# Kernel tuning notes

Measured on AMD Instinct MI355X. Metric: run time of the kernel, lower is better.

Reference implementation:

```python
import jax, jax.numpy as jnp
import numpy as np

N = 50000          # nodes per node type
E = 1_600_000      # edges per canonical etype (avg degree 32)
IN_F = 385         # BERT_EMBEDDING_DIM(384) + NUMERICAL_FEATURES(1)
H = 128            # HIDDEN_DIM
# ntype order: 0=Policy, 1=Control, 2=ComplianceRequirement, 3=Risk
# etypes (src_ntype, dst_ntype): implements, mitigates, violates, addresses, informs
ETYPES = [(0, 1), (1, 3), (3, 2), (0, 2), (2, 0)]


def setup_inputs() -> dict:
    key = jax.random.key(0)
    ks = jax.random.split(key, 12)
    inp = {}
    names = ["feat_policy", "feat_control", "feat_compliance", "feat_risk"]
    for i, n in enumerate(names):
        inp[n] = jax.random.normal(ks[i], (N, IN_F), jnp.float32)
    inp["src"] = jax.random.randint(ks[4], (5, E), 0, N, jnp.int32)
    inp["dst"] = jax.random.randint(ks[5], (5, E), 0, N, jnp.int32)
    s_in = 1.0 / np.sqrt(IN_F).astype(np.float32)
    s_h = np.sqrt(6.0 / (H + H)).astype(np.float32)  # xavier_uniform for GraphConv
    inp["Wp"] = jax.random.uniform(ks[6], (4, IN_F, H), jnp.float32, -s_in, s_in)
    inp["bp"] = jax.random.uniform(ks[7], (4, H), jnp.float32, -s_in, s_in)
    inp["Wc1"] = jax.random.uniform(ks[8], (5, H, H), jnp.float32, -s_h, s_h)
    inp["bc1"] = jnp.zeros((5, H), jnp.float32)
    inp["Wc2"] = jax.random.uniform(ks[9], (5, H, H), jnp.float32, -s_h, s_h)
    inp["bc2"] = jnp.zeros((5, H), jnp.float32)
    return inp


def _graph_conv(x, s, d, W, b):
    """DGL GraphConv(norm='both'): D_dst^{-1/2} A D_src^{-1/2} X W + b."""
    ones = jnp.ones(s.shape[0], x.dtype)
    deg_out = jnp.clip(jax.ops.segment_sum(ones, s, num_segments=N), 1.0)
    deg_in = jnp.clip(jax.ops.segment_sum(ones, d, num_segments=N), 1.0)
    xs = x * jax.lax.rsqrt(deg_out)[:, None]            # [N, H] scale by src out-deg
    agg = jax.ops.segment_sum(xs[s], d, num_segments=N)  # gather + scatter-sum [N, H]
    agg = agg * jax.lax.rsqrt(deg_in)[:, None]
    return agg @ W + b


def reference(feat_policy, feat_control, feat_compliance, feat_risk,
              src, dst, Wp, bp, Wc1, bc1, Wc2, bc2):
    feats = [feat_policy, feat_control, feat_compliance, feat_risk]
    # input projections + relu per node type
    h = [jax.nn.relu(f @ Wp[i] + bp[i]) for i, f in enumerate(feats)]

    def hetero_layer(h, Wc, bc):
        out = [jnp.zeros((N, H), h[0].dtype) for _ in range(4)]
        for k, (st, dt) in enumerate(ETYPES):  # HeteroGraphConv aggregate='sum'
            out[dt] = out[dt] + _graph_conv(h[st], src[k], dst[k], Wc[k], bc[k])
        return out

    h = [jax.nn.relu(v) for v in hetero_layer(h, Wc1, bc1)]
    h = [jax.nn.relu(v) for v in hetero_layer(h, Wc2, bc2)]
    return jnp.stack(h)  # [4, N, H] final embeddings per node type
```

## Files before the change

kernel.cpp:

```cpp
#include <hip/hip_runtime.h>
#include <hip/hip_bf16.h>

#define INF 385
#define HD 128
#define NWG 16
#define HIST_BLOCKS (10 * NWG)

typedef __attribute__((ext_vector_type(8))) short short8;
typedef __attribute__((ext_vector_type(4))) float f32x4;

__device__ inline unsigned short f2b(float f) {
    __hip_bfloat16 h = __float2bfloat16(f);
    return *reinterpret_cast<unsigned short*>(&h);
}
__device__ inline float b2f(unsigned int lo16) {
    union { unsigned int u; float f; } c; c.u = lo16 << 16; return c.f;
}

__device__ __forceinline__ void convert_body(
    const float* f0, const float* f1, const float* f2, const float* f3,
    unsigned int* featB, float* alast, int N, int gid, int nthr)
{
    int per = N * 192;
    int tot = 4 * per;
    for (int p = gid; p < tot; p += nthr) {
        int t = p / per, rem = p - t * per;
        int n = rem / 192, c2 = (rem - n * 192) * 2;
        const float* f = (t < 2) ? (t == 0 ? f0 : f1) : (t == 2 ? f2 : f3);
        const float* row = f + (size_t)n * INF;
        float a = row[c2], b = row[c2 + 1];
        featB[p] = ((unsigned int)f2b(b) << 16) | f2b(a);
    }
    for (int p = gid; p < 4 * N; p += nthr) {
        int t = p / N, n = p - t * N;
        const float* f = (t < 2) ? (t == 0 ? f0 : f1) : (t == 2 ? f2 : f3);
        alast[p] = f[(size_t)n * INF + 384];
    }
}

__global__ __launch_bounds__(1024) void hist_conv_kernel(
    const int* __restrict__ src_all, const int* __restrict__ dst_all,
    unsigned short* __restrict__ partial,
    unsigned short* __restrict__ rank_local,
    int E, int N,
    const float* __restrict__ f0, const float* __restrict__ f1,
    const float* __restrict__ f2, const float* __restrict__ f3,
    unsigned int* __restrict__ featB, float* __restrict__ alast)
{
    __shared__ unsigned int cnt[25000];
    int tid = threadIdx.x;
    if (blockIdx.x >= HIST_BLOCKS) {
        int nconv = gridDim.x - HIST_BLOCKS;
        convert_body(f0, f1, f2, f3, featB, alast, N,
                     (blockIdx.x - HIST_BLOCKS) * 1024 + tid, nconv * 1024);
        return;
    }
    int g = blockIdx.x / NWG;
    int w = blockIdx.x % NWG;
    int half = (N + 1) / 2;
    for (int i = tid; i < half; i += 1024) cnt[i] = 0;
    __syncthreads();

    int C = (E + NWG - 1) / NWG;
    int lo = w * C, hi = min(lo + C, E);
    if (g < 5) {
        const int* arr = dst_all + (size_t)g * E;
        for (int e = lo + tid; e < hi; e += 1024) {
            int d = __builtin_nontemporal_load(&arr[e]);
            unsigned int sh = (d & 1) * 16;
            unsigned int old = atomicAdd(&cnt[d >> 1], 1u << sh);
            rank_local[(size_t)g * E + e] = (unsigned short)((old >> sh) & 0xffffu);
        }
    } else {
        const int* arr = src_all + (size_t)(g - 5) * E;
        for (int e = lo + tid; e < hi; e += 1024) {
            int d = __builtin_nontemporal_load(&arr[e]);
            atomicAdd(&cnt[d >> 1], 1u << ((d & 1) * 16));
        }
    }
    __syncthreads();
    unsigned short* outp = partial + ((size_t)g * NWG + w) * N;
    for (int n = tid; n < N; n += 1024)
        outp[n] = (unsigned short)((cnt[n >> 1] >> ((n & 1) * 16)) & 0xffffu);
}

__global__ void reduce_kernel(unsigned short* __restrict__ partial, int* __restrict__ cnt_dst,
                              float* __restrict__ rsq_out, float* __restrict__ rsq_in, int N) {
    int i = blockIdx.x * blockDim.x + threadIdx.x;
    int stride = gridDim.x * blockDim.x;
    int tot = 10 * N;
    for (; i < tot; i += stride) {
        int g = i / N, n = i - g * N;
        unsigned short* p = partial + ((size_t)g * NWG) * N + n;
        int sum = 0;
        #pragma unroll
        for (int w = 0; w < NWG; ++w) {
            int v = p[(size_t)w * N];
            p[(size_t)w * N] = (unsigned short)sum;
            sum += v;
        }
        float r = rsqrtf((float)max(sum, 1));
        if (g < 5) { cnt_dst[i] = sum; rsq_in[i] = r; }
        else rsq_out[i - 5 * N] = r;
    }
}

__global__ __launch_bounds__(1024) void scan_kernel(const int* __restrict__ cnt_all,
                                                    int* __restrict__ off_all, int n) {
    const int* cnt = cnt_all + (size_t)blockIdx.x * n;
    int* off = off_all + (size_t)blockIdx.x * (n + 1);
    __shared__ int ssum[1024];
    int t = threadIdx.x;
    int chunk = (n + 1023) / 1024;
    int lo = t * chunk, hi = min(lo + chunk, n);
    int s = 0;
    for (int i = lo; i < hi; ++i) s += cnt[i];
    ssum[t] = s;
    __syncthreads();
    for (int d = 1; d < 1024; d <<= 1) {
        int v = (t >= d) ? ssum[t - d] : 0;
        __syncthreads();
        ssum[t] += v;
        __syncthreads();
    }
    int excl = (t == 0) ? 0 : ssum[t - 1];
    for (int i = lo; i < hi; ++i) { off[i] = excl; excl += cnt[i]; }
    if (t == 1023) off[n] = ssum[1023];
}

__global__ void permute_kernel(const int* __restrict__ src_all, const int* __restrict__ dst_all,
                               const int* __restrict__ off, const unsigned short* __restrict__ partial,
                               const unsigned short* __restrict__ rank_local,
                               unsigned short* __restrict__ sorted, int E, int N) {
    int i = blockIdx.x * blockDim.x + threadIdx.x;
    int nthr = gridDim.x * blockDim.x;
    int tot = 5 * E;
    int C = (E + NWG - 1) / NWG;
    for (; i < tot; i += nthr) {
        int k = i / E, e = i - k * E;
        int w = e / C;
        int d = __builtin_nontemporal_load(&dst_all[i]);
        int s = __builtin_nontemporal_load(&src_all[i]);
        int rl = __builtin_nontemporal_load(&rank_local[i]);
        int pos = off[(size_t)k * (N + 1) + d]
                + partial[((size_t)k * NWG + w) * N + d]
                + rl;
        __builtin_nontemporal_store((unsigned short)s, &sorted[(size_t)k * E + pos]);
    }
}

__global__ void convert_kernel(const float* __restrict__ f0, const float* __restrict__ f1,
                               const float* __restrict__ f2, const float* __restrict__ f3,
                               unsigned int* __restrict__ featB, float* __restrict__ alast, int N) {
    convert_body(f0, f1, f2, f3, featB, alast, N,
                 blockIdx.x * blockDim.x + threadIdx.x, gridDim.x * blockDim.x);
}

__global__ void prep_weights_kernel(const float* __restrict__ Wp,
                                    const float* __restrict__ Wc1, const float* __restrict__ Wc2,
                                    const float* __restrict__ bc1, const float* __restrict__ bc2,
                                    unsigned short* __restrict__ WpT,
                                    unsigned short* __restrict__ WcT,
                                    float* __restrict__ cbias) {
    int i = blockIdx.x * blockDim.x + threadIdx.x;
    int stride = gridDim.x * blockDim.x;
    const int nWp = 4 * 128 * 384;
    for (int p = i; p < nWp; p += stride) {
        int t = p / (128 * 384), rem = p % (128 * 384);
        int c = rem / 384, k = rem % 384;
        WpT[p] = f2b(Wp[(size_t)t * INF * HD + (size_t)k * HD + c]);
    }
    const int nWc = 5 * 128 * 128;
    for (int p = i; p < 2 * nWc; p += stride) {
        int layer = p / nWc, rem = p % nWc;
        int e = rem / (128 * 128), rem2 = rem % (128 * 128);
        int c = rem2 / 128, k = rem2 % 128;
        const float* W = layer ? Wc2 : Wc1;
        WcT[p] = f2b(W[(size_t)e * 128 * 128 + (size_t)k * 128 + c]);
    }
    for (int p = i; p < 2 * 4 * 128; p += stride) {
        int layer = p / 512, rem = p % 512;
        int t = rem / 128, c = rem % 128;
        const float* bc = layer ? bc2 : bc1;
        float v;
        if (t == 0) v = bc[4 * 128 + c];
        else if (t == 1) v = bc[0 * 128 + c];
        else if (t == 2) v = bc[2 * 128 + c] + bc[3 * 128 + c];
        else v = bc[1 * 128 + c];
        cbias[p] = v;
    }
}

struct GemmDesc {
    const unsigned short* A;
    const unsigned short* Bt;
    const float* bias;
    const float* rowscale;
    const float* alast;
    const float* wlast;
    unsigned short* out;
};
struct GemmBatch { GemmDesc d[5]; };

__global__ __launch_bounds__(256) void gemm_mfma_kernel(
    GemmBatch batch, int lda, int M, int K, int relu)
{
    const GemmDesc dsc = batch.d[blockIdx.y];
    const unsigned short* __restrict__ Bt = dsc.Bt;
    const unsigned short* __restrict__ A = dsc.A;

    __shared__ __align__(16) unsigned short As[64][72];
    __shared__ __align__(16) unsigned short Bs[128][72];
    const int tid = threadIdx.x;
    const int bm = blockIdx.x * 64;
    const int wid = tid >> 6, lane = tid & 63;
    const int wr = wid & 1, wc = wid >> 1;
    const int l15 = lane & 15, l4 = lane >> 4;

    f32x4 acc[2][4] = {};

    for (int k0 = 0; k0 < K; k0 += 64) {
        {
            int r = tid >> 2, q = tid & 3;
            int gm = bm + r;
            if (gm < M) {
                const uint4* g = (const uint4*)(A + (size_t)gm * lda + k0 + q * 16);
                *(uint4*)&As[r][q * 16] = g[0];
                *(uint4*)&As[r][q * 16 + 8] = g[1];
            } else {
                uint4 z = {0, 0, 0, 0};
                *(uint4*)&As[r][q * 16] = z;
                *(uint4*)&As[r][q * 16 + 8] = z;
            }
        }
        {
            int col = tid >> 1, hf = tid & 1;
            const uint4* g = (const uint4*)(Bt + (size_t)col * K + k0 + hf * 32);
            #pragma unroll
            for (int j = 0; j < 4; ++j)
                *(uint4*)&Bs[col][hf * 32 + j * 8] = g[j];
        }
        __syncthreads();
        #pragma unroll
        for (int kk = 0; kk < 2; ++kk) {
            short8 a[2], b[4];
            #pragma unroll
            for (int mi = 0; mi < 2; ++mi)
                a[mi] = *(const short8*)&As[wr * 32 + mi * 16 + l15][kk * 32 + l4 * 8];
            #pragma unroll
            for (int ni = 0; ni < 4; ++ni)
                b[ni] = *(const short8*)&Bs[wc * 64 + ni * 16 + l15][kk * 32 + l4 * 8];
            #pragma unroll
            for (int mi = 0; mi < 2; ++mi)
                #pragma unroll
                for (int ni = 0; ni < 4; ++ni)
                    acc[mi][ni] = __builtin_amdgcn_mfma_f32_16x16x32_bf16(
                        a[mi], b[ni], acc[mi][ni], 0, 0, 0);
        }
        __syncthreads();
    }

    #pragma unroll
    for (int mi = 0; mi < 2; ++mi) {
        #pragma unroll
        for (int r = 0; r < 4; ++r) {
            int grow = bm + wr * 32 + mi * 16 + l4 * 4 + r;
            if (grow >= M) continue;
            float rs = dsc.rowscale ? dsc.rowscale[grow] : 1.f;
            float al = dsc.alast ? dsc.alast[grow] : 0.f;
            #pragma unroll
            for (int ni = 0; ni < 4; ++ni) {
                int gcol = wc * 64 + ni * 16 + l15;
                float v = acc[mi][ni][r];
                if (dsc.wlast) v += al * dsc.wlast[gcol];
                if (dsc.bias) v += dsc.bias[gcol];
                v *= rs;
                if (relu) v = fmaxf(v, 0.f);
                dsc.out[(size_t)grow * HD + gcol] = f2b(v);
            }
        }
    }
}

struct GatherDesc {
    const unsigned short* msgA; const unsigned short* sortedA;
    const int* offA; const float* rsqA;
    const unsigned short* msgB; const unsigned short* sortedB;
    const int* offB; const float* rsqB;
    const float* bias; void* out;
};
struct GatherBatch { GatherDesc d[4]; };

__device__ __forceinline__ void gather_seg(
    const unsigned short* __restrict__ msg, const unsigned short* __restrict__ sorted,
    int beg, int end, size_t loff, float& ax, float& ay)
{
    int e = beg;
    for (; e + 16 <= end; e += 16) {
        int s[16];
        unsigned int v[16];
        #pragma unroll
        for (int j = 0; j < 16; ++j) s[j] = sorted[e + j];
        #pragma unroll
        for (int j = 0; j < 16; ++j)
            v[j] = *(const unsigned int*)(msg + (size_t)s[j] * HD + loff);
        #pragma unroll
        for (int j = 0; j < 16; ++j) {
            ax += b2f(v[j] & 0xffffu);
            ay += b2f(v[j] >> 16);
        }
    }
    if (e + 8 <= end) {
        int s[8];
        unsigned int v[8];
        #pragma unroll
        for (int j = 0; j < 8; ++j) s[j] = sorted[e + j];
        #pragma unroll
        for (int j = 0; j < 8; ++j)
            v[j] = *(const unsigned int*)(msg + (size_t)s[j] * HD + loff);
        #pragma unroll
        for (int j = 0; j < 8; ++j) {
            ax += b2f(v[j] & 0xffffu);
            ay += b2f(v[j] >> 16);
        }
        e += 8;
    }
    for (; e < end; ++e) {
        int s0 = sorted[e];
        unsigned int v0 = *(const unsigned int*)(msg + (size_t)s0 * HD + loff);
        ax += b2f(v0 & 0xffffu);
        ay += b2f(v0 >> 16);
    }
}

template<int OUT_BF16>
__global__ __launch_bounds__(256) void gather_kernel(GatherBatch batch, int n)
{
    const GatherDesc d = batch.d[blockIdx.y];
    int node = blockIdx.x * 4 + (threadIdx.x >> 6);
    if (node >= n) return;
    int lane = threadIdx.x & 63;
    const size_t loff = (size_t)lane * 2;

    float ox, oy;
    {
        float ax = 0.f, ay = 0.f;
        gather_seg(d.msgA, d.sortedA, d.offA[node], d.offA[node + 1], loff, ax, ay);
        float r = d.rsqA[node];
        ox = ax * r; oy = ay * r;
    }
    if (d.msgB) {
        float bx = 0.f, by = 0.f;
        gather_seg(d.msgB, d.sortedB, d.offB[node], d.offB[node + 1], loff, bx, by);
        float r = d.rsqB[node];
        ox += bx * r; oy += by * r;
    }
    float2 bv = *(const float2*)(d.bias + loff);
    ox = fmaxf(ox + bv.x, 0.f);
    oy = fmaxf(oy + bv.y, 0.f);
    if (OUT_BF16) {
        unsigned int packed = ((unsigned int)f2b(oy) << 16) | f2b(ox);
        ((unsigned int*)d.out)[(size_t)node * (HD / 2) + lane] = packed;
    } else {
        float2 o = {ox, oy};
        ((float2*)d.out)[(size_t)node * (HD / 2) + lane] = o;
    }
}

extern "C" void kernel_launch(void* const* d_in, const int* in_sizes, int n_in,
                              void* d_out, int out_size, void* d_ws, size_t ws_size,
                              hipStream_t stream)
{
    const float* feat[4] = {(const float*)d_in[0], (const float*)d_in[1],
                            (const float*)d_in[2], (const float*)d_in[3]};
    const int* src_all = (const int*)d_in[4];
    const int* dst_all = (const int*)d_in[5];
    const float* Wp  = (const float*)d_in[6];
    const float* bp  = (const float*)d_in[7];
    const float* Wc1 = (const float*)d_in[8];
    const float* bc1 = (const float*)d_in[9];
    const float* Wc2 = (const float*)d_in[10];
    const float* bc2 = (const float*)d_in[11];

    const int N = in_sizes[0] / INF;
    const int E = in_sizes[4] / 5;

    const int st_[5] = {0, 1, 3, 0, 2};

    char* w = (char*)d_ws;
    auto take = [&](size_t bytes) { char* p = w; w += (bytes + 255) & ~(size_t)255; return p; };
    int*   cnt_dst = (int*)take(5 * (size_t)N * 4);
    float* rsq_out = (float*)take(5 * (size_t)N * 4);
    float* rsq_in  = (float*)take(5 * (size_t)N * 4);
    int*   off     = (int*)take(5 * (size_t)(N + 1) * 4);
    unsigned short* sorted = (unsigned short*)take(5 * (size_t)E * 2);
    float* alast   = (float*)take(4 * (size_t)N * 4);
    unsigned short* WpT = (unsigned short*)take(4 * 128 * 384 * 2);
    unsigned short* WcT = (unsigned short*)take(2 * 5 * 128 * 128 * 2);
    float* cbias   = (float*)take(2 * 4 * 128 * 4);

    const size_t pr_bytes = 10u * NWG * (size_t)N * 2 + 5 * (size_t)E * 2;
    const size_t blob_sz = 4 * (size_t)N * 384 * 2;
    size_t fixed_used = (size_t)(w - (char*)d_ws);
    bool roomy = ws_size >= fixed_used + pr_bytes + blob_sz + (1u << 20);

    unsigned short *partial, *rank_local, *featB, *msg;
    if (roomy) {
        partial    = (unsigned short*)take(10u * NWG * (size_t)N * 2);
        rank_local = (unsigned short*)take(5 * (size_t)E * 2);
        char* blob = (char*)take(blob_sz);
        featB = (unsigned short*)blob;
        msg   = (unsigned short*)blob;
    } else {
        char* blob = (char*)take(blob_sz);
        partial    = (unsigned short*)blob;
        rank_local = (unsigned short*)(blob + 10u * NWG * (size_t)N * 2);
        featB      = (unsigned short*)blob;
        msg        = (unsigned short*)(blob + 32u * 1024 * 1024);
    }
    unsigned short* h0 = (unsigned short*)d_out;
    unsigned short* h1 = (unsigned short*)d_out + 4 * (size_t)N * HD;

    const int gblk = (N + 63) / 64;

    prep_weights_kernel<<<512, 256, 0, stream>>>(Wp, Wc1, Wc2, bc1, bc2, WpT, WcT, cbias);

    hist_conv_kernel<<<roomy ? HIST_BLOCKS + 512 : HIST_BLOCKS, 1024, 0, stream>>>(
        src_all, dst_all, partial, rank_local, E, N,
        feat[0], feat[1], feat[2], feat[3], (unsigned int*)featB, alast);
    reduce_kernel<<<(10 * N + 255) / 256, 256, 0, stream>>>(partial, cnt_dst, rsq_out, rsq_in, N);
    scan_kernel<<<5, 1024, 0, stream>>>(cnt_dst, off, N);
    permute_kernel<<<2048, 256, 0, stream>>>(src_all, dst_all, off, partial, rank_local,
                                             sorted, E, N);
    if (!roomy)
        convert_kernel<<<2048, 256, 0, stream>>>(feat[0], feat[1], feat[2], feat[3],
                                                 (unsigned int*)featB, alast, N);

    {
        GemmBatch pb = {};
        for (int t = 0; t < 4; ++t) {
            pb.d[t].A = featB + (size_t)t * N * 384;
            pb.d[t].Bt = WpT + (size_t)t * 128 * 384;
            pb.d[t].bias = bp + (size_t)t * HD;
            pb.d[t].rowscale = nullptr;
            pb.d[t].alast = alast + (size_t)t * N;
            pb.d[t].wlast = Wp + (size_t)t * INF * HD + 384 * HD;
            pb.d[t].out = h0 + (size_t)t * N * HD;
        }
        gemm_mfma_kernel<<<dim3(gblk, 4), 256, 0, stream>>>(pb, 384, N, 384, 1);
    }

    for (int layer = 0; layer < 2; ++layer) {
        const unsigned short* hin = layer ? h1 : h0;
        const unsigned short* WT = WcT + (size_t)layer * 5 * 128 * 128;
        const float* cb = cbias + (size_t)layer * 4 * 128;

        {
            GemmBatch cbch = {};
            for (int k = 0; k < 5; ++k) {
                cbch.d[k].A = hin + (size_t)st_[k] * N * HD;
                cbch.d[k].Bt = WT + (size_t)k * 128 * 128;
                cbch.d[k].bias = nullptr;
                cbch.d[k].rowscale = rsq_out + (size_t)k * N;
                cbch.d[k].alast = nullptr;
                cbch.d[k].wlast = nullptr;
                cbch.d[k].out = msg + (size_t)k * N * HD;
            }
            gemm_mfma_kernel<<<dim3(gblk, 5), 256, 0, stream>>>(cbch, HD, N, 128, 0);
        }

        {
            auto S = [&](int k) { return sorted + (size_t)k * E; };
            auto O = [&](int k) { return off + (size_t)k * (N + 1); };
            auto R = [&](int k) { return rsq_in + (size_t)k * N; };
            auto M_ = [&](int k) { return msg + (size_t)k * N * HD; };
            const int ksA[4] = {0, 1, 2, 4};
            const int dt [4] = {1, 3, 2, 0};
            GatherBatch gb = {};
            for (int y = 0; y < 4; ++y) {
                int k = ksA[y];
                gb.d[y].msgA = M_(k); gb.d[y].sortedA = S(k);
                gb.d[y].offA = O(k);  gb.d[y].rsqA = R(k);
                gb.d[y].msgB = nullptr; gb.d[y].sortedB = nullptr;
                gb.d[y].offB = nullptr; gb.d[y].rsqB = nullptr;
                gb.d[y].bias = cb + (size_t)dt[y] * HD;
                if (layer == 0)
                    gb.d[y].out = h1 + (size_t)dt[y] * N * HD;
                else
                    gb.d[y].out = (float*)d_out + (size_t)dt[y] * N * HD;
            }
            gb.d[2].msgB = M_(3); gb.d[2].sortedB = S(3);
            gb.d[2].offB = O(3);  gb.d[2].rsqB = R(3);
            const int gg = (N + 3) / 4;
            if (layer == 0)
                gather_kernel<1><<<dim3(gg, 4), 256, 0, stream>>>(gb, N);
            else
                gather_kernel<0><<<dim3(gg, 4), 256, 0, stream>>>(gb, N);
        }
    }
}
```

Before: 1.120 ms.

## Vectorize gather to 16-byte loads across four edge subgroups; XCD-aware permute

The gather kernel now splits each wavefront into four 16-lane subgroups. Each lane loads 16 bytes (8 bf16 values) of a neighbour row, so four edges are processed in parallel per wave, and the partial sums are then reduced with cross-lane shuffles. The goal is fewer, wider memory requests per gathered row and better memory-level parallelism. The permute kernel assigns edge types to blocks by XCD index so each edge type's offset and partial tables stay in one XCD's cache, and it drops the nontemporal store. The costs are extra shuffle work, idle lanes in the epilogue, and an uneven split of blocks across edge types.

```diff
diff --git a/kernel.cpp b/kernel.cpp
--- a/kernel.cpp
+++ b/kernel.cpp
@@ -128,24 +128,37 @@
     if (t == 1023) off[n] = ssum[1023];
 }
 
-__global__ void permute_kernel(const int* __restrict__ src_all, const int* __restrict__ dst_all,
-                               const int* __restrict__ off, const unsigned short* __restrict__ partial,
-                               const unsigned short* __restrict__ rank_local,
-                               unsigned short* __restrict__ sorted, int E, int N) {
-    int i = blockIdx.x * blockDim.x + threadIdx.x;
-    int nthr = gridDim.x * blockDim.x;
-    int tot = 5 * E;
+__global__ __launch_bounds__(256) void permute_kernel(
+    const int* __restrict__ src_all, const int* __restrict__ dst_all,
+    const int* __restrict__ off, const unsigned short* __restrict__ partial,
+    const unsigned short* __restrict__ rank_local,
+    unsigned short* __restrict__ sorted, int E, int N)
+{
+    int b = blockIdx.x;
+    int xcd = b & 7;
+    int k = (xcd < 5) ? xcd : xcd - 5;
+    int sub = (xcd >= 5) ? 1 : 0;
+    int nGroups = (k < 3) ? 2 : 1;
+    int blocksPerXcd = gridDim.x >> 3;
+    int tid_in_xcd = (b >> 3) * 256 + threadIdx.x;
+    int e = sub * (blocksPerXcd * 256) + tid_in_xcd;
+    int nthr = nGroups * blocksPerXcd * 256;
     int C = (E + NWG - 1) / NWG;
-    for (; i < tot; i += nthr) {
-        int k = i / E, e = i - k * E;
+
+    const int* dsts = dst_all + (size_t)k * E;
+    const int* srcs = src_all + (size_t)k * E;
+    const unsigned short* rl = rank_local + (size_t)k * E;
+    const int* offk = off + (size_t)k * (N + 1);
+    const unsigned short* pk = partial + (size_t)k * NWG * N;
+    unsigned short* sk = sorted + (size_t)k * E;
+
+    for (; e < E; e += nthr) {
         int w = e / C;
-        int d = __builtin_nontemporal_load(&dst_all[i]);
-        int s = __builtin_nontemporal_load(&src_all[i]);
-        int rl = __builtin_nontemporal_load(&rank_local[i]);
-        int pos = off[(size_t)k * (N + 1) + d]
-                + partial[((size_t)k * NWG + w) * N + d]
-                + rl;
-        __builtin_nontemporal_store((unsigned short)s, &sorted[(size_t)k * E + pos]);
+        int d = __builtin_nontemporal_load(&dsts[e]);
+        int s = __builtin_nontemporal_load(&srcs[e]);
+        int r = __builtin_nontemporal_load(&rl[e]);
+        int pos = offk[d] + pk[(size_t)w * N + d] + r;
+        sk[pos] = (unsigned short)s;
     }
 }
 
@@ -291,45 +304,39 @@
 };
 struct GatherBatch { GatherDesc d[4]; };
 
+__device__ __forceinline__ void accum8(uint4 v, float* acc) {
+    acc[0] += b2f(v.x & 0xffffu); acc[1] += b2f(v.x >> 16);
+    acc[2] += b2f(v.y & 0xffffu); acc[3] += b2f(v.y >> 16);
+    acc[4] += b2f(v.z & 0xffffu); acc[5] += b2f(v.z >> 16);
+    acc[6] += b2f(v.w & 0xffffu); acc[7] += b2f(v.w >> 16);
+}
+
 __device__ __forceinline__ void gather_seg(
     const unsigned short* __restrict__ msg, const unsigned short* __restrict__ sorted,
-    int beg, int end, size_t loff, float& ax, float& ay)
-{
+    int beg, int end, int sub, int lbyte, float* acc)
+{
+    const char* mbase = (const char*)msg;
     int e = beg;
     for (; e + 16 <= end; e += 16) {
-        int s[16];
-        unsigned int v[16];
-        #pragma unroll
-        for (int j = 0; j < 16; ++j) s[j] = sorted[e + j];
-        #pragma unroll
-        for (int j = 0; j < 16; ++j)
-            v[j] = *(const unsigned int*)(msg + (size_t)s[j] * HD + loff);
-        #pragma unroll
-        for (int j = 0; j < 16; ++j) {
-            ax += b2f(v[j] & 0xffffu);
-            ay += b2f(v[j] >> 16);
-        }
-    }
-    if (e + 8 <= end) {
-        int s[8];
-        unsigned int v[8];
-        #pragma unroll
-        for (int j = 0; j < 8; ++j) s[j] = sorted[e + j];
-        #pragma unroll
-        for (int j = 0; j < 8; ++j)
-            v[j] = *(const unsigned int*)(msg + (size_t)s[j] * HD + loff);
-        #pragma unroll
-        for (int j = 0; j < 8; ++j) {
-            ax += b2f(v[j] & 0xffffu);
-            ay += b2f(v[j] >> 16);
-        }
-        e += 8;
-    }
-    for (; e < end; ++e) {
-        int s0 = sorted[e];
-        unsigned int v0 = *(const unsigned int*)(msg + (size_t)s0 * HD + loff);
-        ax += b2f(v0 & 0xffffu);
-        ay += b2f(v0 >> 16);
+        uint4 v[4];
+        #pragma unroll
+        for (int r = 0; r < 4; ++r) {
+            int s = sorted[e + r * 4 + sub];
+            v[r] = *(const uint4*)(mbase + (size_t)s * 256 + lbyte);
+        }
+        #pragma unroll
+        for (int r = 0; r < 4; ++r) accum8(v[r], acc);
+    }
+    if (e < end) {
+        #pragma unroll
+        for (int r = 0; r < 4; ++r) {
+            int idx = e + r * 4 + sub;
+            if (idx < end) {
+                int s = sorted[idx];
+                uint4 v = *(const uint4*)(mbase + (size_t)s * 256 + lbyte);
+                accum8(v, acc);
+            }
+        }
     }
 }
 
@@ -340,30 +347,52 @@
     int node = blockIdx.x * 4 + (threadIdx.x >> 6);
     if (node >= n) return;
     int lane = threadIdx.x & 63;
-    const size_t loff = (size_t)lane * 2;
-
-    float ox, oy;
+    int sub = lane >> 4;
+    int l16 = lane & 15;
+    int lbyte = l16 * 16;
+
+    float comb[8];
     {
-        float ax = 0.f, ay = 0.f;
-        gather_seg(d.msgA, d.sortedA, d.offA[node], d.offA[node + 1], loff, ax, ay);
-        float r = d.rsqA[node];
-        ox = ax * r; oy = ay * r;
-    }
-    if (d.msgB) {
-        float bx = 0.f, by = 0.f;
-        gather_seg(d.msgB, d.sortedB, d.offB[node], d.offB[node + 1], loff, bx, by);
-        float r = d.rsqB[node];
-        ox += bx * r; oy += by * r;
-    }
-    float2 bv = *(const float2*)(d.bias + loff);
-    ox = fmaxf(ox + bv.x, 0.f);
-    oy = fmaxf(oy + bv.y, 0.f);
-    if (OUT_BF16) {
-        unsigned int packed = ((unsigned int)f2b(oy) << 16) | f2b(ox);
-        ((unsigned int*)d.out)[(size_t)node * (HD / 2) + lane] = packed;
-    } else {
-        float2 o = {ox, oy};
-        ((float2*)d.out)[(size_t)node * (HD / 2) + lane] = o;
+        float acc[8] = {};
+        gather_seg(d.msgA, d.sortedA, d.offA[node], d.offA[node + 1], sub, lbyte, acc);
+        float rA = d.rsqA[node];
+        if (d.msgB) {
+            float acc2[8] = {};
+            gather_seg(d.msgB, d.sortedB, d.offB[node], d.offB[node + 1], sub, lbyte, acc2);
+            float rB = d.rsqB[node];
+            #pragma unroll
+            for (int c = 0; c < 8; ++c) comb[c] = acc[c] * rA + acc2[c] * rB;
+        } else {
+            #pragma unroll
+            for (int c = 0; c < 8; ++c) comb[c] = acc[c] * rA;
+        }
+    }
+    #pragma unroll
+    for (int c = 0; c < 8; ++c) {
+        comb[c] += __shfl_xor(comb[c], 16);
+        comb[c] += __shfl_xor(comb[c], 32);
+    }
+    if (sub == 0) {
+        const float* bptr = d.bias + l16 * 8;
+        float4 b0 = *(const float4*)bptr;
+        float4 b1 = *(const float4*)(bptr + 4);
+        float o[8] = {comb[0] + b0.x, comb[1] + b0.y, comb[2] + b0.z, comb[3] + b0.w,
+                      comb[4] + b1.x, comb[5] + b1.y, comb[6] + b1.z, comb[7] + b1.w};
+        #pragma unroll
+        for (int c = 0; c < 8; ++c) o[c] = fmaxf(o[c], 0.f);
+        if (OUT_BF16) {
+            uint4 pv;
+            pv.x = ((unsigned int)f2b(o[1]) << 16) | f2b(o[0]);
+            pv.y = ((unsigned int)f2b(o[3]) << 16) | f2b(o[2]);
+            pv.z = ((unsigned int)f2b(o[5]) << 16) | f2b(o[4]);
+            pv.w = ((unsigned int)f2b(o[7]) << 16) | f2b(o[6]);
+            *(uint4*)((char*)d.out + (size_t)node * 256 + lbyte) = pv;
+        } else {
+            float4 f0 = {o[0], o[1], o[2], o[3]};
+            float4 f1 = {o[4], o[5], o[6], o[7]};
+            float4* op = (float4*)((char*)d.out + (size_t)node * 512 + (size_t)l16 * 32);
+            op[0] = f0; op[1] = f1;
+        }
     }
 }
 
```

Result: slower. 1.151 ms (+2.8%).
